# Performance work log

Hardware: AMD Instinct MI355X
Metric: run time of the kernel (lower is better)

The kernel has to match this reference:

```python
import jax, jax.numpy as jnp
import numpy as np

D = 256        # d_model
NH = 8         # num_head
NL = 4         # num_level
KS = 8         # kernel_size (even)
K2 = KS * KS
HD = D // NH   # head_dim
LEVELS = [(128, 128), (64, 64), (32, 32), (16, 16)]


def _kernel_indices():
    # even kernel: linspace(-KS/2+0.5, KS/2-0.5, KS), meshgrid ij, stack [j,i] (x,y), / KS
    idx = np.linspace(-KS // 2 + 0.5, KS // 2 - 0.5, KS).astype(np.float32)
    i, j = np.meshgrid(idx, idx, indexing='ij')
    return jnp.asarray(np.stack([j, i], axis=-1).reshape(-1, 2) / KS)  # [K2, 2]


def setup_inputs():
    key = jax.random.key(0)
    ks = jax.random.split(key, 12)
    b, q = 2, 300
    l2 = sum(h * w for h, w in LEVELS)
    query = jax.random.normal(ks[0], (b, q, D), jnp.float32)
    value = jax.random.normal(ks[1], (b, l2, D), jnp.float32)
    v_shape = np.array(LEVELS, dtype=np.int64)                      # [NL, 2] (H, W)
    starts = np.concatenate([[0], np.cumsum([h * w for h, w in LEVELS])[:-1]])
    v_start_index = starts.astype(np.int64)                          # [NL]
    v_mask = jnp.zeros((b, l2), dtype=bool)                          # no padding
    v_valid_ratios = jnp.ones((b, 1, 1, NL, 1, 2), jnp.float32)
    center = jax.random.uniform(ks[2], (b, q, 2), jnp.float32, 0.25, 0.75)
    size = jax.random.uniform(ks[3], (b, q, 2), jnp.float32, 0.05, 0.25)
    ref_windows = jnp.concatenate([center, size], axis=-1)           # [b, q, 4] cx,cy,w,h
    s = 0.02
    Wv = s * jax.random.normal(ks[4], (D, D), jnp.float32)
    bv = jnp.zeros((D,), jnp.float32)
    Wbox = s * jax.random.normal(ks[5], (NH * NL * 4, D), jnp.float32)
    bbox = jax.random.uniform(ks[6], (NH * NL * 4,), jnp.float32)    # uniform init per _reset_parameters
    Wattn = s * jax.random.normal(ks[7], (NH * NL * 4, D), jnp.float32)
    battn = s * jax.random.normal(ks[8], (NH * NL * 4,), jnp.float32)
    Wout = s * jax.random.normal(ks[9], (D, D), jnp.float32)
    bout = jnp.zeros((D,), jnp.float32)
    return dict(query=query, value=value, v_shape=v_shape, v_mask=v_mask,
                v_start_index=v_start_index, v_valid_ratios=v_valid_ratios,
                ref_windows=ref_windows, Wv=Wv, bv=bv, Wbox=Wbox, bbox=bbox,
                Wattn=Wattn, battn=battn, Wout=Wout, bout=bout,
                kernel_indices=_kernel_indices())


def reference(query, value, v_shape, v_mask, v_start_index, v_valid_ratios,
              ref_windows, Wv, bv, Wbox, bbox, Wattn, battn, Wout, bout,
              kernel_indices):
    b, q, _ = query.shape
    # value projection + mask fill
    val = jnp.einsum('bnd,ed->bne', value, Wv) + bv
    val = jnp.where(v_mask[..., None], 0.0, val)
    val = val.reshape(b, -1, NH, HD)                                 # [b, l2, NH, HD]

    # attention logits: base 2x2 grid expanded to KSxKS via repeat_interleave
    aw = (jnp.einsum('bqd,od->bqo', query, Wattn) + battn).reshape(b, q, NH, NL, 2, 2)
    aw = jnp.repeat(jnp.repeat(aw, KS // 2, axis=-1), KS // 2, axis=-2)  # [b,q,NH,NL,KS,KS]
    spatial = jax.nn.softmax(aw.reshape(b, q, NH, NL * K2), axis=-1).reshape(b, q, NH, NL, K2)
    level = jax.nn.softmax(aw, axis=3).reshape(b, q, NH, NL, K2)

    # sampling grid (_where_to_attend)
    ob = (jnp.einsum('bqd,od->bqo', query, Wbox) + bbox).reshape(b, q, NH, NL, 4)
    rw = ref_windows[:, :, None, None, :]                            # [b,q,1,1,4]
    boxes = rw + ob / 8.0 * rw[..., jnp.array([2, 3, 2, 3])]
    center = boxes[..., None, :2]                                    # [b,q,NH,NL,1,2]
    size = boxes[..., None, 2:]
    grid = center + kernel_indices * jax.nn.relu(size)               # [b,q,NH,NL,K2,2]
    grid = grid * v_valid_ratios

    # multi-level bilinear sampling (grid_sample, align_corners=False, zero padding)
    bi = jnp.arange(b)[:, None, None, None]
    hi = jnp.arange(NH)[None, None, :, None]
    sampled = []
    for lv in range(NL):
        Hl = int(v_shape[lv, 0]); Wl = int(v_shape[lv, 1]); st = int(v_start_index[lv])
        vl = val[:, st:st + Hl * Wl]                                 # [b, Hl*Wl, NH, HD]
        loc = grid[:, :, :, lv]                                      # [b,q,NH,K2,2]
        x = loc[..., 0] * Wl - 0.5
        y = loc[..., 1] * Hl - 0.5
        x0 = jnp.floor(x); y0 = jnp.floor(y)
        dx = x - x0; dy = y - y0
        acc = jnp.zeros((b, q, NH, K2, HD), val.dtype)
        for ix, iy, w in ((x0, y0, (1 - dx) * (1 - dy)),
                          (x0 + 1, y0, dx * (1 - dy)),
                          (x0, y0 + 1, (1 - dx) * dy),
                          (x0 + 1, y0 + 1, dx * dy)):
            valid = (ix >= 0) & (ix < Wl) & (iy >= 0) & (iy < Hl)
            idx = (jnp.clip(iy, 0, Hl - 1) * Wl + jnp.clip(ix, 0, Wl - 1)).astype(jnp.int32)
            v4 = vl[bi, idx, hi]                                     # [b,q,NH,K2,HD]
            acc = acc + jnp.where(valid, w, 0.0)[..., None] * v4
        sampled.append(acc)
    sampled = jnp.stack(sampled, axis=3)                             # [b,q,NH,NL,K2,HD]

    # box-attention output: spatial softmax over all (level, point)
    out = jnp.einsum('bqhlkd,bqhlk->bqhd', sampled, spatial).reshape(b, q, D)
    out = jnp.einsum('bqd,od->bqo', out, Wout) + bout
    # instance mask output: level softmax per kernel point
    mask = jnp.einsum('bqhlkd,bqhlk->bqkhd', sampled, level).reshape(b, q, K2, D)
    mask = jnp.einsum('bqkd,od->bqko', mask, Wout) + bout
    return out, mask
```

## Files before the change

kernel.cpp:

```cpp
#include <hip/hip_runtime.h>
#include <cstdint>
#include <cstddef>

typedef unsigned short u16;
typedef unsigned int   u32;
typedef __attribute__((ext_vector_type(8))) short bf16x8;
typedef __attribute__((ext_vector_type(4))) float f32x4;

static constexpr int kQ = 300;
static constexpr int kL2 = 21760;

__device__ __forceinline__ u16 bf16_rne(float f) {
    u32 u = __float_as_uint(f);
    u += 0x7FFFu + ((u >> 16) & 1u);
    return (u16)(u >> 16);
}
__device__ __forceinline__ u32 pack2(float lo, float hi) {
    return (u32)bf16_rne(lo) | ((u32)bf16_rne(hi) << 16);
}
__device__ __forceinline__ float lo16(u32 u) { return __uint_as_float(u << 16); }
__device__ __forceinline__ float hi16(u32 u) { return __uint_as_float(u & 0xFFFF0000u); }

__global__ __launch_bounds__(256)
void convert_weights(const float* __restrict__ Wv, u16* __restrict__ Wv_b,
                     const float* __restrict__ Wout, u16* __restrict__ Wout_b)
{
    const float* src = (blockIdx.x < 32) ? Wv : Wout;
    u16* dst = (blockIdx.x < 32) ? Wv_b : Wout_b;
    int i = ((blockIdx.x & 31) * 256 + threadIdx.x) * 8;
    float4 a = *(const float4*)(src + i);
    float4 b = *(const float4*)(src + i + 4);
    uint4 o;
    o.x = pack2(a.x, a.y); o.y = pack2(a.z, a.w);
    o.z = pack2(b.x, b.y); o.w = pack2(b.z, b.w);
    *(uint4*)(dst + i) = o;
}

template<bool A_F32, bool OUT_BF16>
__global__ __launch_bounds__(256)
void gemm_bf16(const void* __restrict__ Aptr, const u16* __restrict__ W,
               const float* __restrict__ bias, void* __restrict__ Cout,
               const unsigned char* __restrict__ rowmask)
{
    __shared__ u16 S[8192];
    u16* As = S;
    u16* Bs = S + 4096;
    const int tid = threadIdx.x;
    const int m0 = blockIdx.x * 128;
    const int n0 = blockIdx.y * 128;
    const int lane = tid & 63;
    const int w = tid >> 6;
    const int wm = w & 1, wn = w >> 1;
    const int g = lane >> 4, r = lane & 15;

    f32x4 acc[4][4];
#pragma unroll
    for (int i = 0; i < 4; i++)
#pragma unroll
        for (int j = 0; j < 4; j++)
            acc[i][j] = (f32x4){0.f, 0.f, 0.f, 0.f};

    for (int kt = 0; kt < 8; ++kt) {
        const int k0 = kt * 32;
#pragma unroll
        for (int i = 0; i < 2; ++i) {
            int c = tid + i * 256;
            int row = c & 127, gg = c >> 7;
            if (A_F32) {
                const float* p = (const float*)Aptr + (size_t)(m0 + row) * 256 + k0 + gg * 8;
                float4 a0 = *(const float4*)p;
                float4 a1 = *(const float4*)(p + 4);
                uint4 o;
                o.x = pack2(a0.x, a0.y); o.y = pack2(a0.z, a0.w);
                o.z = pack2(a1.x, a1.y); o.w = pack2(a1.z, a1.w);
                *(uint4*)(As + ((size_t)c << 3)) = o;
            } else {
                uint4 va = *(const uint4*)((const u16*)Aptr + (size_t)(m0 + row) * 256 + k0 + gg * 8);
                *(uint4*)(As + ((size_t)c << 3)) = va;
            }
            uint4 vb = *(const uint4*)(W + (size_t)(n0 + row) * 256 + k0 + gg * 8);
            *(uint4*)(Bs + ((size_t)c << 3)) = vb;
        }
        __syncthreads();
        bf16x8 af[4], bf[4];
#pragma unroll
        for (int mf = 0; mf < 4; ++mf)
            af[mf] = *(const bf16x8*)(As + ((g * 128 + wm * 64 + mf * 16 + r) << 3));
#pragma unroll
        for (int nf = 0; nf < 4; ++nf)
            bf[nf] = *(const bf16x8*)(Bs + ((g * 128 + wn * 64 + nf * 16 + r) << 3));
#pragma unroll
        for (int mf = 0; mf < 4; ++mf)
#pragma unroll
            for (int nf = 0; nf < 4; ++nf)
                acc[mf][nf] = __builtin_amdgcn_mfma_f32_16x16x32_bf16(
                    af[mf], bf[nf], acc[mf][nf], 0, 0, 0);
        __syncthreads();
    }

    if (!OUT_BF16) {
        float* C = (float*)Cout;
#pragma unroll
        for (int nf = 0; nf < 4; ++nf) {
            int ng = n0 + wn * 64 + nf * 16 + r;
            float bb = bias[ng];
#pragma unroll
            for (int mf = 0; mf < 4; ++mf) {
                int mg = m0 + wm * 64 + mf * 16 + g * 4;
#pragma unroll
                for (int reg = 0; reg < 4; ++reg) {
                    float z = 1.f;
                    if (rowmask && rowmask[mg + reg]) z = 0.f;
                    C[(size_t)(mg + reg) * 256 + ng] = (acc[mf][nf][reg] + bb) * z;
                }
            }
        }
    } else {
        u16* C = (u16*)Cout;
#pragma unroll
        for (int round = 0; round < 2; ++round) {
            __syncthreads();
            if (wn == round) {
#pragma unroll
                for (int nf = 0; nf < 4; ++nf) {
                    int col = nf * 16 + r;
                    float bb = bias[n0 + round * 64 + col];
#pragma unroll
                    for (int mf = 0; mf < 4; ++mf) {
                        int row0 = wm * 64 + mf * 16 + g * 4;
#pragma unroll
                        for (int reg = 0; reg < 4; ++reg) {
                            float z = 1.f;
                            if (rowmask && rowmask[m0 + row0 + reg]) z = 0.f;
                            S[(row0 + reg) * 64 + col] =
                                bf16_rne((acc[mf][nf][reg] + bb) * z);
                        }
                    }
                }
            }
            __syncthreads();
            int row = tid >> 1, hb = tid & 1;
            const u16* src = S + row * 64 + hb * 32;
            u16* dst = C + (size_t)(m0 + row) * 256 + n0 + round * 64 + hb * 32;
#pragma unroll
            for (int j = 0; j < 4; ++j)
                ((uint4*)dst)[j] = ((const uint4*)src)[j];
        }
    }
}

__global__ __launch_bounds__(256)
void gemm_out_fused(const float* __restrict__ out_part, const float* __restrict__ W,
                    const float* __restrict__ bias, float* __restrict__ C, int M)
{
    __shared__ float As[32][68];
    __shared__ float Ws[32][68];
    const int tid = threadIdx.x;
    const int m0 = blockIdx.x * 64;
    const int n0 = blockIdx.y * 64;
    const int tx = tid & 15, ty = tid >> 4;
    float acc[4][4] = {};

    for (int k0 = 0; k0 < 256; k0 += 32) {
#pragma unroll
        for (int i = 0; i < 2; i++) {
            int t = tid + i * 256;
            int rr = t >> 3;
            int c4 = (t & 7) << 2;
            int ra = min(m0 + rr, M - 1);
            const float* p = out_part + (size_t)(4 * ra) * 256 + k0 + c4;
            float4 v0 = *(const float4*)p;
            float4 v1 = *(const float4*)(p + 256);
            float4 v2 = *(const float4*)(p + 512);
            float4 v3 = *(const float4*)(p + 768);
            float4 va;
            va.x = (v0.x + v1.x) + (v2.x + v3.x);
            va.y = (v0.y + v1.y) + (v2.y + v3.y);
            va.z = (v0.z + v1.z) + (v2.z + v3.z);
            va.w = (v0.w + v1.w) + (v2.w + v3.w);
            As[c4 + 0][rr] = va.x; As[c4 + 1][rr] = va.y;
            As[c4 + 2][rr] = va.z; As[c4 + 3][rr] = va.w;
            float4 vw = *(const float4*)(W + (size_t)(n0 + rr) * 256 + k0 + c4);
            Ws[c4 + 0][rr] = vw.x; Ws[c4 + 1][rr] = vw.y;
            Ws[c4 + 2][rr] = vw.z; Ws[c4 + 3][rr] = vw.w;
        }
        __syncthreads();
#pragma unroll
        for (int kk = 0; kk < 32; kk++) {
            float4 a = *(const float4*)&As[kk][ty * 4];
            float4 wv4 = *(const float4*)&Ws[kk][tx * 4];
            float av[4] = {a.x, a.y, a.z, a.w};
            float wv[4] = {wv4.x, wv4.y, wv4.z, wv4.w};
#pragma unroll
            for (int i = 0; i < 4; i++)
#pragma unroll
                for (int j = 0; j < 4; j++)
                    acc[i][j] += av[i] * wv[j];
        }
        __syncthreads();
    }
#pragma unroll
    for (int i = 0; i < 4; i++) {
        int rr = m0 + ty * 4 + i;
        if (rr >= M) continue;
        int n = n0 + tx * 4;
        float4 o;
        o.x = acc[i][0] + bias[n + 0];
        o.y = acc[i][1] + bias[n + 1];
        o.z = acc[i][2] + bias[n + 2];
        o.w = acc[i][3] + bias[n + 3];
        *(float4*)(C + (size_t)rr * 256 + n) = o;
    }
}

__global__ __launch_bounds__(256)
void param_kernel(const float* __restrict__ query,
                  const float* __restrict__ Wattn, const float* __restrict__ battn,
                  const float* __restrict__ Wbox,  const float* __restrict__ bbox,
                  const float* __restrict__ ref_windows,
                  const float* __restrict__ vvr,
                  float* __restrict__ params)
{
    __shared__ float qrow[256];
    __shared__ float awob[256];
    __shared__ float4 boxs[8][4];
    __shared__ float wgts[8][4][4];
    __shared__ float cqds[8][4];

    const int bq = blockIdx.x;
    const int b = bq / kQ;
    const int tid = threadIdx.x;

    if (tid < 64)
        ((float4*)qrow)[tid] = ((const float4*)(query + (size_t)bq * 256))[tid];
    __syncthreads();

    {
        const float* Wrow = (tid < 128) ? (Wattn + (size_t)tid * 256)
                                        : (Wbox + (size_t)(tid - 128) * 256);
        float s = (tid < 128) ? battn[tid] : bbox[tid - 128];
#pragma unroll 8
        for (int d4 = 0; d4 < 64; d4++) {
            float4 wv = ((const float4*)Wrow)[d4];
            float4 qv = ((const float4*)qrow)[d4];
            s += wv.x * qv.x + wv.y * qv.y + wv.z * qv.z + wv.w * qv.w;
        }
        awob[tid] = s;
    }
    __syncthreads();

    if (tid < 8) {
        const int h = tid;
        float m = -1e30f;
        float E[16];
#pragma unroll
        for (int i = 0; i < 16; i++) m = fmaxf(m, awob[h * 16 + i]);
        float Ssum = 0.f;
#pragma unroll
        for (int i = 0; i < 16; i++) { E[i] = expf(awob[h * 16 + i] - m); Ssum += E[i]; }
        float invS16 = 1.f / (16.f * Ssum);
#pragma unroll
        for (int qd = 0; qd < 4; qd++) {
            float Sq = E[qd] + E[4 + qd] + E[8 + qd] + E[12 + qd];
            float inv = 1.f / Sq;
#pragma unroll
            for (int l = 0; l < 4; l++) wgts[h][l][qd] = E[l * 4 + qd] * inv;
            cqds[h][qd] = Sq * invS16;
        }
    }
    if (tid >= 64 && tid < 96) {
        const int t = tid - 64;
        const int h = t >> 2, l = t & 3;
        float4 rw = ((const float4*)ref_windows)[bq];
        float ob0 = awob[128 + h * 16 + l * 4 + 0];
        float ob1 = awob[128 + h * 16 + l * 4 + 1];
        float ob2 = awob[128 + h * 16 + l * 4 + 2];
        float ob3 = awob[128 + h * 16 + l * 4 + 3];
        float cx = rw.x + ob0 * 0.125f * rw.z;
        float cy = rw.y + ob1 * 0.125f * rw.w;
        float sx = fmaxf(rw.z + ob2 * 0.125f * rw.z, 0.f);
        float sy = fmaxf(rw.w + ob3 * 0.125f * rw.w, 0.f);
        float vrx = vvr[(b * 4 + l) * 2 + 0];
        float vry = vvr[(b * 4 + l) * 2 + 1];
        boxs[h][l] = make_float4(cx * vrx, cy * vry, sx * vrx, sy * vry);
    }
    __syncthreads();

    float* p = params + (size_t)bq * 288;
    if (tid < 32)       ((float4*)p)[tid] = ((float4*)boxs)[tid];
    else if (tid < 64)  ((float4*)p)[tid] = ((float4*)wgts)[tid - 32];
    else if (tid < 72)  ((float4*)p)[tid] = ((float4*)cqds)[tid - 64];
}

__global__ __launch_bounds__(512)
void sample_bf16(const u16* __restrict__ valb,
                 const float* __restrict__ params,
                 u16* __restrict__ maskb,
                 float* __restrict__ out_part)
{
    __shared__ float4 boxs[8][4];
    __shared__ float wgts[8][4][4];
    __shared__ float cqds[8][4];
    __shared__ float warr[8][256];

    const int blk = blockIdx.x;
    const int bq = blk >> 2;
    const int kq = blk & 3;
    const int b = bq / kQ;
    const int tid = threadIdx.x;

    if (tid < 72) {
        float4 v = ((const float4*)(params + (size_t)bq * 288))[tid];
        if (tid < 32)      ((float4*)boxs)[tid] = v;
        else if (tid < 64) ((float4*)wgts)[tid - 32] = v;
        else               ((float4*)cqds)[tid - 64] = v;
    }
    __syncthreads();

    const int klocal = tid >> 5;
    const int h = (tid >> 2) & 7;
    const int ch = tid & 3;
    const int k = kq * 16 + klocal;
    const float kx = (float)(k & 7) * 0.125f - 0.4375f;
    const float ky = (float)(k >> 3) * 0.125f - 0.4375f;
    const int qd = (((k >> 5) & 1) << 1) | ((k >> 2) & 1);

    float acc[8];
#pragma unroll
    for (int e = 0; e < 8; e++) acc[e] = 0.f;

    static constexpr int LW[4]  = {128, 64, 32, 16};
    static constexpr int LST[4] = {0, 16384, 20480, 21504};

#pragma unroll
    for (int l = 0; l < 4; l++) {
        const int Wl = LW[l];
        const u16* vbase = valb + ((size_t)(b * kL2 + LST[l]) << 8) + h * 32 + ch * 8;
        float4 bx = boxs[h][l];
        float lw = wgts[h][l][qd];
        float x = (bx.x + kx * bx.z) * Wl - 0.5f;
        float y = (bx.y + ky * bx.w) * Wl - 0.5f;
        float x0f = floorf(x), y0f = floorf(y);
        float dx = x - x0f, dy = y - y0f;
        int x0 = (int)x0f, y0 = (int)y0f;
        int x1 = x0 + 1, y1 = y0 + 1;
        int x0c = min(max(x0, 0), Wl - 1), x1c = min(max(x1, 0), Wl - 1);
        int y0c = min(max(y0, 0), Wl - 1), y1c = min(max(y1, 0), Wl - 1);
        float vx0 = (x0 >= 0 && x0 < Wl) ? 1.f : 0.f;
        float vx1 = (x1 >= 0 && x1 < Wl) ? 1.f : 0.f;
        float vy0 = (y0 >= 0 && y0 < Wl) ? 1.f : 0.f;
        float vy1 = (y1 >= 0 && y1 < Wl) ? 1.f : 0.f;
        float w00 = (1.f - dx) * (1.f - dy) * vx0 * vy0 * lw;
        float w10 = dx * (1.f - dy) * vx1 * vy0 * lw;
        float w01 = (1.f - dx) * dy * vx0 * vy1 * lw;
        float w11 = dx * dy * vx1 * vy1 * lw;
        uint4 v00 = *(const uint4*)(vbase + ((size_t)(y0c * Wl + x0c) << 8));
        uint4 v10 = *(const uint4*)(vbase + ((size_t)(y0c * Wl + x1c) << 8));
        uint4 v01 = *(const uint4*)(vbase + ((size_t)(y1c * Wl + x0c) << 8));
        uint4 v11 = *(const uint4*)(vbase + ((size_t)(y1c * Wl + x1c) << 8));
        acc[0] += w00*lo16(v00.x) + w10*lo16(v10.x) + w01*lo16(v01.x) + w11*lo16(v11.x);
        acc[1] += w00*hi16(v00.x) + w10*hi16(v10.x) + w01*hi16(v01.x) + w11*hi16(v11.x);
        acc[2] += w00*lo16(v00.y) + w10*lo16(v10.y) + w01*lo16(v01.y) + w11*lo16(v11.y);
        acc[3] += w00*hi16(v00.y) + w10*hi16(v10.y) + w01*hi16(v01.y) + w11*hi16(v11.y);
        acc[4] += w00*lo16(v00.z) + w10*lo16(v10.z) + w01*lo16(v01.z) + w11*lo16(v11.z);
        acc[5] += w00*hi16(v00.z) + w10*hi16(v10.z) + w01*hi16(v01.z) + w11*hi16(v11.z);
        acc[6] += w00*lo16(v00.w) + w10*lo16(v10.w) + w01*lo16(v01.w) + w11*lo16(v11.w);
        acc[7] += w00*hi16(v00.w) + w10*hi16(v10.w) + w01*hi16(v01.w) + w11*hi16(v11.w);
    }

    {
        uint4 o;
        o.x = pack2(acc[0], acc[1]);
        o.y = pack2(acc[2], acc[3]);
        o.z = pack2(acc[4], acc[5]);
        o.w = pack2(acc[6], acc[7]);
        *(uint4*)(maskb + (((size_t)bq * 64 + k) << 8) + h * 32 + ch * 8) = o;
    }

    {
        const int wave = tid >> 6;
        const int lane = tid & 63;
        float c = cqds[h][qd];
#pragma unroll
        for (int e = 0; e < 8; e++) {
            float v = acc[e] * c;
            v += __shfl_xor(v, 32);
            if (lane < 32) warr[wave][h * 32 + ch * 8 + e] = v;
        }
    }
    __syncthreads();
    if (tid < 256) {
        float s = 0.f;
#pragma unroll
        for (int wv = 0; wv < 8; wv++) s += warr[wv][tid];
        out_part[(size_t)blk * 256 + tid] = s;
    }
}

extern "C" void kernel_launch(void* const* d_in, const int* in_sizes, int n_in,
                              void* d_out, int out_size, void* d_ws, size_t ws_size,
                              hipStream_t stream)
{
    const float* query       = (const float*)d_in[0];
    const float* value       = (const float*)d_in[1];
    const unsigned char* v_mask = (const unsigned char*)d_in[3];
    const float* vvr         = (const float*)d_in[5];
    const float* ref_windows = (const float*)d_in[6];
    const float* Wv    = (const float*)d_in[7];
    const float* bv    = (const float*)d_in[8];
    const float* Wbox  = (const float*)d_in[9];
    const float* bbox  = (const float*)d_in[10];
    const float* Wattn = (const float*)d_in[11];
    const float* battn = (const float*)d_in[12];
    const float* Wout  = (const float*)d_in[13];
    const float* bout  = (const float*)d_in[14];

    char* wsp = (char*)d_ws;
    u16* Wv_b    = (u16*)wsp;                 wsp += (size_t)65536 * 2;
    u16* Wout_b  = (u16*)wsp;                 wsp += (size_t)65536 * 2;
    u16* val_b   = (u16*)wsp;                 wsp += (size_t)11141120 * 2;
    u16* mask_b  = (u16*)wsp;                 wsp += (size_t)9830400 * 2;
    float* params   = (float*)wsp;            wsp += (size_t)600 * 288 * 4;
    float* out_part = (float*)wsp;            wsp += (size_t)2400 * 256 * 4;

    float* out  = (float*)d_out;
    float* mask = out + (size_t)600 * 256;

    convert_weights<<<64, 256, 0, stream>>>(Wv, Wv_b, Wout, Wout_b);
    param_kernel<<<600, 256, 0, stream>>>(query, Wattn, battn, Wbox, bbox,
                                          ref_windows, vvr, params);
    gemm_bf16<true, true><<<dim3(340, 2), 256, 0, stream>>>(value, Wv_b, bv, val_b, v_mask);
    sample_bf16<<<2400, 512, 0, stream>>>(val_b, params, mask_b, out_part);
    gemm_bf16<false, false><<<dim3(300, 2), 256, 0, stream>>>(mask_b, Wout_b, bout, mask, nullptr);
    gemm_out_fused<<<dim3(10, 4), 256, 0, stream>>>(out_part, Wout, bout, out, 600);
}
```

Baseline: 147.6 us.

## Double-buffer GEMM LDS with register prefetch, swizzle, and halve M tile

The bf16 GEMM used for the value projection and the mask output projection now prefetches the next K-slice into registers while MFMAs run on the current LDS buffer. It double-buffers shared memory, which removes one barrier per iteration. LDS row indices are rotated (a swizzle) to reduce bank conflicts on fragment reads. The M tile is cut from 128 to 64 rows, doubling the grid to raise occupancy and block count, at the cost of reloading W more often and using more LDS per block.

```diff
diff --git a/kernel.cpp b/kernel.cpp
--- a/kernel.cpp
+++ b/kernel.cpp
@@ -36,77 +36,97 @@
     *(uint4*)(dst + i) = o;
 }
 
+#define GLOAD(kt) { \
+    const int k0 = (kt) * 32; \
+    if constexpr (A_F32) { \
+        const float* p = (const float*)Aptr + (size_t)(m0 + arow) * 256 + k0 + asub * 8; \
+        ra0 = *(const float4*)p; ra1 = *(const float4*)(p + 4); \
+    } else { \
+        rav = *(const uint4*)((const u16*)Aptr + (size_t)(m0 + arow) * 256 + k0 + asub * 8); \
+    } \
+    rb0 = *(const uint4*)(W + (size_t)(n0 + b0row) * 256 + k0 + bsub * 8); \
+    rb1 = *(const uint4*)(W + (size_t)(n0 + b1row) * 256 + k0 + bsub * 8); }
+
+#define GSTORE(buf) { \
+    u16* As = S + (buf) * 6144; \
+    u16* Bs = As + 2048; \
+    const int ac = asub * 64 + ((arow + 2 * asub) & 63); \
+    if constexpr (A_F32) { \
+        uint4 o; \
+        o.x = pack2(ra0.x, ra0.y); o.y = pack2(ra0.z, ra0.w); \
+        o.z = pack2(ra1.x, ra1.y); o.w = pack2(ra1.z, ra1.w); \
+        *(uint4*)(As + (ac << 3)) = o; \
+    } else { \
+        *(uint4*)(As + (ac << 3)) = rav; \
+    } \
+    *(uint4*)(Bs + ((bsub * 128 + ((b0row + 2 * bsub) & 127)) << 3)) = rb0; \
+    *(uint4*)(Bs + ((bsub * 128 + ((b1row + 2 * bsub) & 127)) << 3)) = rb1; }
+
 template<bool A_F32, bool OUT_BF16>
 __global__ __launch_bounds__(256)
 void gemm_bf16(const void* __restrict__ Aptr, const u16* __restrict__ W,
                const float* __restrict__ bias, void* __restrict__ Cout,
                const unsigned char* __restrict__ rowmask)
 {
-    __shared__ u16 S[8192];
-    u16* As = S;
-    u16* Bs = S + 4096;
+    __shared__ u16 S[12288];
     const int tid = threadIdx.x;
-    const int m0 = blockIdx.x * 128;
+    const int m0 = blockIdx.x * 64;
     const int n0 = blockIdx.y * 128;
     const int lane = tid & 63;
     const int w = tid >> 6;
     const int wm = w & 1, wn = w >> 1;
     const int g = lane >> 4, r = lane & 15;
 
-    f32x4 acc[4][4];
-#pragma unroll
-    for (int i = 0; i < 4; i++)
+    const int arow = tid >> 2, asub = tid & 3;
+    const int b0row = tid >> 2;
+    const int b1row = 64 + (tid >> 2);
+    const int bsub = tid & 3;
+
+    f32x4 acc[2][4];
+#pragma unroll
+    for (int i = 0; i < 2; i++)
 #pragma unroll
         for (int j = 0; j < 4; j++)
             acc[i][j] = (f32x4){0.f, 0.f, 0.f, 0.f};
 
+    float4 ra0, ra1; uint4 rav; uint4 rb0, rb1;
+
+    GLOAD(0);
+    GSTORE(0);
     for (int kt = 0; kt < 8; ++kt) {
-        const int k0 = kt * 32;
-#pragma unroll
-        for (int i = 0; i < 2; ++i) {
-            int c = tid + i * 256;
-            int row = c & 127, gg = c >> 7;
-            if (A_F32) {
-                const float* p = (const float*)Aptr + (size_t)(m0 + row) * 256 + k0 + gg * 8;
-                float4 a0 = *(const float4*)p;
-                float4 a1 = *(const float4*)(p + 4);
-                uint4 o;
-                o.x = pack2(a0.x, a0.y); o.y = pack2(a0.z, a0.w);
-                o.z = pack2(a1.x, a1.y); o.w = pack2(a1.z, a1.w);
-                *(uint4*)(As + ((size_t)c << 3)) = o;
-            } else {
-                uint4 va = *(const uint4*)((const u16*)Aptr + (size_t)(m0 + row) * 256 + k0 + gg * 8);
-                *(uint4*)(As + ((size_t)c << 3)) = va;
-            }
-            uint4 vb = *(const uint4*)(W + (size_t)(n0 + row) * 256 + k0 + gg * 8);
-            *(uint4*)(Bs + ((size_t)c << 3)) = vb;
-        }
+        if (kt < 7) GLOAD(kt + 1);
         __syncthreads();
-        bf16x8 af[4], bf[4];
-#pragma unroll
-        for (int mf = 0; mf < 4; ++mf)
-            af[mf] = *(const bf16x8*)(As + ((g * 128 + wm * 64 + mf * 16 + r) << 3));
-#pragma unroll
-        for (int nf = 0; nf < 4; ++nf)
-            bf[nf] = *(const bf16x8*)(Bs + ((g * 128 + wn * 64 + nf * 16 + r) << 3));
-#pragma unroll
-        for (int mf = 0; mf < 4; ++mf)
+        const u16* As = S + (kt & 1) * 6144;
+        const u16* Bs = As + 2048;
+        bf16x8 af[2], bf[4];
+#pragma unroll
+        for (int mf = 0; mf < 2; ++mf) {
+            int X = wm * 32 + mf * 16 + r;
+            af[mf] = *(const bf16x8*)(As + ((g * 64 + ((X + 2 * g) & 63)) << 3));
+        }
+#pragma unroll
+        for (int nf = 0; nf < 4; ++nf) {
+            int X = wn * 64 + nf * 16 + r;
+            bf[nf] = *(const bf16x8*)(Bs + ((g * 128 + ((X + 2 * g) & 127)) << 3));
+        }
+#pragma unroll
+        for (int mf = 0; mf < 2; ++mf)
 #pragma unroll
             for (int nf = 0; nf < 4; ++nf)
                 acc[mf][nf] = __builtin_amdgcn_mfma_f32_16x16x32_bf16(
                     af[mf], bf[nf], acc[mf][nf], 0, 0, 0);
-        __syncthreads();
-    }
-
-    if (!OUT_BF16) {
+        if (kt < 7) GSTORE((kt + 1) & 1);
+    }
+
+    if constexpr (!OUT_BF16) {
         float* C = (float*)Cout;
 #pragma unroll
         for (int nf = 0; nf < 4; ++nf) {
             int ng = n0 + wn * 64 + nf * 16 + r;
             float bb = bias[ng];
 #pragma unroll
-            for (int mf = 0; mf < 4; ++mf) {
-                int mg = m0 + wm * 64 + mf * 16 + g * 4;
+            for (int mf = 0; mf < 2; ++mf) {
+                int mg = m0 + wm * 32 + mf * 16 + g * 4;
 #pragma unroll
                 for (int reg = 0; reg < 4; ++reg) {
                     float z = 1.f;
@@ -126,8 +146,8 @@
                     int col = nf * 16 + r;
                     float bb = bias[n0 + round * 64 + col];
 #pragma unroll
-                    for (int mf = 0; mf < 4; ++mf) {
-                        int row0 = wm * 64 + mf * 16 + g * 4;
+                    for (int mf = 0; mf < 2; ++mf) {
+                        int row0 = wm * 32 + mf * 16 + g * 4;
 #pragma unroll
                         for (int reg = 0; reg < 4; ++reg) {
                             float z = 1.f;
@@ -139,12 +159,13 @@
                 }
             }
             __syncthreads();
-            int row = tid >> 1, hb = tid & 1;
-            const u16* src = S + row * 64 + hb * 32;
-            u16* dst = C + (size_t)(m0 + row) * 256 + n0 + round * 64 + hb * 32;
-#pragma unroll
-            for (int j = 0; j < 4; ++j)
-                ((uint4*)dst)[j] = ((const uint4*)src)[j];
+#pragma unroll
+            for (int i = 0; i < 2; ++i) {
+                int c = tid + i * 256;
+                int row = c >> 3, cc = c & 7;
+                *(uint4*)(C + (size_t)(m0 + row) * 256 + n0 + round * 64 + cc * 8) =
+                    *(const uint4*)(S + row * 64 + cc * 8);
+            }
         }
     }
 }
@@ -429,8 +450,8 @@
     convert_weights<<<64, 256, 0, stream>>>(Wv, Wv_b, Wout, Wout_b);
     param_kernel<<<600, 256, 0, stream>>>(query, Wattn, battn, Wbox, bbox,
                                           ref_windows, vvr, params);
-    gemm_bf16<true, true><<<dim3(340, 2), 256, 0, stream>>>(value, Wv_b, bv, val_b, v_mask);
+    gemm_bf16<true, true><<<dim3(680, 2), 256, 0, stream>>>(value, Wv_b, bv, val_b, v_mask);
     sample_bf16<<<2400, 512, 0, stream>>>(val_b, params, mask_b, out_part);
-    gemm_bf16<false, false><<<dim3(300, 2), 256, 0, stream>>>(mask_b, Wout_b, bout, mask, nullptr);
+    gemm_bf16<false, false><<<dim3(600, 2), 256, 0, stream>>>(mask_b, Wout_b, bout, mask, nullptr);
     gemm_out_fused<<<dim3(10, 4), 256, 0, stream>>>(out_part, Wout, bout, out, 600);
 }
```

New measurement: 129.7 us. 1.14x faster.
